# Kernel tuning notes

Measured on AMD Instinct MI355X. Metric: run time of the kernel, lower is better.

## Reference

```python
import jax, jax.numpy as jnp
import numpy as np

B, O, A, H, Z = 4096, 512, 64, 2048, 256
CLAMP = 10.0


def _lin(x, w, b):
    # torch nn.Linear layout: w [out, in]
    return x @ w.T + b


def setup_inputs() -> dict:
    key = jax.random.key(0)
    ks = jax.random.split(key, 24)
    n = jax.random.normal
    s = 0.02
    inp = {
        'x_t': n(ks[0], (B, O), jnp.float32),
        'a_prev': n(ks[1], (B, A), jnp.float32),
        'h_prev': n(ks[2], (B, H), jnp.float32),
        'eps': n(ks[3], (B, Z), jnp.float32),
        # prior_net: Linear(H,H) -> ReLU -> Linear(H, 2Z)
        'prior_w1': n(ks[4], (H, H), jnp.float32) * s,
        'prior_b1': jnp.zeros((H,), jnp.float32),
        'prior_w2': n(ks[5], (2 * Z, H), jnp.float32) * s,
        'prior_b2': jnp.zeros((2 * Z,), jnp.float32),
        # enc_net: Linear(O+H,H) -> ReLU -> Linear(H, 2Z)
        'enc_w1': n(ks[6], (H, O + H), jnp.float32) * s,
        'enc_b1': jnp.zeros((H,), jnp.float32),
        'enc_w2': n(ks[7], (2 * Z, H), jnp.float32) * s,
        'enc_b2': jnp.zeros((2 * Z,), jnp.float32),
        # dec_net: Linear(Z+H,H) -> ReLU -> Linear(H, 2O)
        'dec_w1': n(ks[8], (H, Z + H), jnp.float32) * s,
        'dec_b1': jnp.zeros((H,), jnp.float32),
        'dec_w2': n(ks[9], (2 * O, H), jnp.float32) * s,
        'dec_b2': jnp.zeros((2 * O,), jnp.float32),
        # GRUCell: input = O + A + Z, gates ordered (r, z, n)
        'w_ih': n(ks[10], (3 * H, O + A + Z), jnp.float32) * s,
        'w_hh': n(ks[11], (3 * H, H), jnp.float32) * s,
        'b_ih': jnp.zeros((3 * H,), jnp.float32),
        'b_hh': jnp.zeros((3 * H,), jnp.float32),
    }
    return inp


def vrnn_step(x_t, a_prev, h_prev, eps,
              prior_w1, prior_b1, prior_w2, prior_b2,
              enc_w1, enc_b1, enc_w2, enc_b2,
              dec_w1, dec_b1, dec_w2, dec_b2,
              w_ih, w_hh, b_ih, b_hh):
    # prior stats from h_prev
    prior_stats = _lin(jax.nn.relu(_lin(h_prev, prior_w1, prior_b1)), prior_w2, prior_b2)
    mu_p, logvar_p = jnp.split(prior_stats, 2, axis=-1)

    # encoder on [x, h]
    enc_stats = _lin(jax.nn.relu(_lin(jnp.concatenate([x_t, h_prev], -1), enc_w1, enc_b1)), enc_w2, enc_b2)
    mu_q, logvar_q = jnp.split(enc_stats, 2, axis=-1)
    logvar_q = jnp.clip(logvar_q, -CLAMP, CLAMP)
    std_q = jnp.exp(0.5 * logvar_q)
    z_t = mu_q + eps * std_q  # reparameterization

    # decoder on [z, h]
    dec_out = _lin(jax.nn.relu(_lin(jnp.concatenate([z_t, h_prev], -1), dec_w1, dec_b1)), dec_w2, dec_b2)
    mu_x, logvar_x = jnp.split(dec_out, 2, axis=-1)
    logvar_x = jnp.clip(logvar_x, -CLAMP, CLAMP)
    nll = 0.5 * jnp.sum((x_t - mu_x) ** 2 * jnp.exp(-logvar_x) + logvar_x, axis=-1)

    # KL(q || p), diagonal Gaussians
    var_p = jnp.exp(logvar_p)
    kl = 0.5 * jnp.sum((mu_q - mu_p) ** 2 / var_p + jnp.exp(logvar_q) / var_p
                       + (logvar_p - logvar_q) - 1.0, axis=-1)

    # GRUCell (torch gate order: r, z, n)
    rnn_in = jnp.concatenate([x_t, z_t, a_prev], -1)
    gi = rnn_in @ w_ih.T + b_ih
    gh = h_prev @ w_hh.T + b_hh
    i_r, i_z, i_n = jnp.split(gi, 3, axis=-1)
    h_r, h_z, h_n = jnp.split(gh, 3, axis=-1)
    r = jax.nn.sigmoid(i_r + h_r)
    zg = jax.nn.sigmoid(i_z + h_z)
    n = jnp.tanh(i_n + r * h_n)
    h_t = (1.0 - zg) * n + zg * h_prev

    return h_t, nll, kl, z_t, mu_q, logvar_q


def reference(x_t, a_prev, h_prev, eps,
              prior_w1, prior_b1, prior_w2, prior_b2,
              enc_w1, enc_b1, enc_w2, enc_b2,
              dec_w1, dec_b1, dec_w2, dec_b2,
              w_ih, w_hh, b_ih, b_hh):
    return vrnn_step(x_t, a_prev, h_prev, eps,
                     prior_w1, prior_b1, prior_w2, prior_b2,
                     enc_w1, enc_b1, enc_w2, enc_b2,
                     dec_w1, dec_b1, dec_w2, dec_b2,
                     w_ih, w_hh, b_ih, b_hh)
```

## Files before the change

### kernel.cpp

```cpp
#include <hip/hip_runtime.h>
#include <stdint.h>


#define B_SZ 4096
#define H_SZ 2048
#define Z_SZ 256

typedef __attribute__((ext_vector_type(4))) float f32x4;
typedef __attribute__((ext_vector_type(8))) short s16x8;

__device__ __forceinline__ uint16_t f2b(float f) {
  union { float f; uint32_t u; } v; v.f = f;
  uint32_t u = v.u;
  uint32_t r = (u + 0x7FFFu + ((u >> 16) & 1u)) >> 16;
  return (uint16_t)r;
}
__device__ __forceinline__ float b2f(uint16_t h) {
  union { uint32_t u; float f; } v; v.u = ((uint32_t)h) << 16; return v.f;
}
__device__ __forceinline__ float clip10(float v) { return fminf(fmaxf(v, -10.0f), 10.0f); }

struct MC {
  const float* src[11];
  uint16_t* dst[11];
  int c8[11];
  int sld[11];
  int dld[11];
  int base[12];
};

__global__ __launch_bounds__(256) void multiconv(MC mc, int nseg, int total) {
  int gid = blockIdx.x * 256 + threadIdx.x;
  if (gid >= total) return;
  int s = 0;
  while (s + 1 < nseg && gid >= mc.base[s + 1]) ++s;
  int local = gid - mc.base[s];
  int c8 = mc.c8[s];
  int row = local / c8;
  int cg = local - row * c8;
  const f32x4* sp = (const f32x4*)(mc.src[s] + (size_t)row * mc.sld[s] + (size_t)cg * 8);
  f32x4 lo = sp[0], hi = sp[1];
  s16x8 p;
  p[0] = (short)f2b(lo[0]); p[1] = (short)f2b(lo[1]);
  p[2] = (short)f2b(lo[2]); p[3] = (short)f2b(lo[3]);
  p[4] = (short)f2b(hi[0]); p[5] = (short)f2b(hi[1]);
  p[6] = (short)f2b(hi[2]); p[7] = (short)f2b(hi[3]);
  *(s16x8*)(mc.dst[s] + (size_t)row * mc.dld[s] + (size_t)cg * 8) = p;
}

__device__ __forceinline__ void gload_lds16(const uint16_t* g, uint16_t* l) {
  __builtin_amdgcn_global_load_lds(
      (const __attribute__((address_space(1))) uint32_t*)g,
      (__attribute__((address_space(3))) uint32_t*)(uintptr_t)(void*)l,
      16, 0, 0);
}

__global__ __launch_bounds__(512, 2)
void gemm8p(const uint16_t* __restrict__ A, int lda,
            const uint16_t* __restrict__ W,
            const float* __restrict__ bias0, const float* __restrict__ bias1,
            uint16_t* __restrict__ C0, int ldc0, int splitN,
            uint16_t* __restrict__ C1, int ldc1,
            int Nt, int K) {
  __shared__ uint16_t Ab[2][2][8192];
  __shared__ uint16_t Bb[2][2][8192];
  const int NT = K >> 6;
  int mtile = blockIdx.x / Nt;
  int ntile = blockIdx.x - mtile * Nt;
  const int brow = mtile << 8, bcol = ntile << 8;
  const int tid = threadIdx.x;
  const int l = tid & 63;
  const int w = tid >> 6;
  const int wr = w >> 2, wcn = w & 3;
  const int fr = l & 15, fq = l >> 4;
  const int sr0 = tid >> 3;
  const int scg = tid & 7;
  const int dstoff = tid * 8;

  f32x4 acc[8][4] = {};

  auto stage_half = [&](int t, int q, int d) {
#pragma unroll
    for (int r = 0; r < 2; ++r) {
      int row = r * 64 + sr0;
      int col = (scg ^ (row & 7)) << 3;
      if (q < 2)
        gload_lds16(A + (size_t)(brow + q * 128 + row) * lda + t * 64 + col,
                    &Ab[d][q][r * 4096 + dstoff]);
      else
        gload_lds16(W + (size_t)(bcol + (q - 2) * 128 + row) * K + t * 64 + col,
                    &Bb[d][q - 2][r * 4096 + dstoff]);
    }
  };

#pragma unroll
  for (int q = 0; q < 4; ++q) stage_half(0, q, 0);

  for (int t = 0; t < NT; ++t) {
    const int d = t & 1;
    const bool more = (t + 1 < NT);
    if (more) {
      stage_half(t + 1, 0, d ^ 1);
      asm volatile("s_waitcnt vmcnt(2)" ::: "memory");
    } else {
      asm volatile("s_waitcnt vmcnt(0)" ::: "memory");
    }
    __builtin_amdgcn_s_barrier();

#pragma unroll
    for (int q = 0; q < 4; ++q) {
      const int mh = q >> 1, nh = q & 1;
      if (q > 0 && more) stage_half(t + 1, q, d ^ 1);
      s16x8 fb[2][2];
#pragma unroll
      for (int nn = 0; nn < 2; ++nn)
#pragma unroll
        for (int ks = 0; ks < 2; ++ks) {
          int row = wcn * 64 + nh * 32 + nn * 16 + fr;
          int half = row >> 7, rl = row & 127;
          fb[nn][ks] = *(const s16x8*)&Bb[d][half]
              [rl * 64 + ((ks * 32 + fq * 8) ^ ((rl & 7) << 3))];
        }
      s16x8 fa[4][2];
#pragma unroll
      for (int mm = 0; mm < 4; ++mm)
#pragma unroll
        for (int ks = 0; ks < 2; ++ks) {
          int rl = mh * 64 + mm * 16 + fr;
          fa[mm][ks] = *(const s16x8*)&Ab[d][wr]
              [rl * 64 + ((ks * 32 + fq * 8) ^ ((rl & 7) << 3))];
        }
      __builtin_amdgcn_s_setprio(1);
#pragma unroll
      for (int mm = 0; mm < 4; ++mm)
#pragma unroll
        for (int nn = 0; nn < 2; ++nn)
#pragma unroll
          for (int ks = 0; ks < 2; ++ks)
            acc[mh * 4 + mm][nh * 2 + nn] = __builtin_amdgcn_mfma_f32_16x16x32_bf16(
                fa[mm][ks], fb[nn][ks], acc[mh * 4 + mm][nh * 2 + nn], 0, 0, 0);
      __builtin_amdgcn_s_setprio(0);
      __builtin_amdgcn_s_barrier();
    }
  }

#pragma unroll
  for (int m = 0; m < 8; ++m) {
    int grow = brow + wr * 128 + m * 16 + fq * 4;
#pragma unroll
    for (int n = 0; n < 4; ++n) {
      int gcol = bcol + wcn * 64 + n * 16 + fr;
      bool first = gcol < splitN;
      float bs = first ? bias0[gcol] : bias1[gcol - splitN];
#pragma unroll
      for (int i = 0; i < 4; ++i) {
        float v = acc[m][n][i] + bs;
        if (first) {
          C0[(size_t)(grow + i) * ldc0 + gcol] = f2b(fmaxf(v, 0.0f));
        } else {
          C1[(size_t)(grow + i) * ldc1 + (gcol - splitN)] = f2b(v);
        }
      }
    }
  }
}

template <int EPI>
__global__ __launch_bounds__(256)
void gemm_bt(const uint16_t* __restrict__ A0, int lda0, int ks1,
             const uint16_t* __restrict__ A1, int lda1, int ks2,
             const uint16_t* __restrict__ A2, int lda2,
             const uint16_t* __restrict__ W,
             const float* __restrict__ bias0, const float* __restrict__ bias1,
             uint16_t* __restrict__ C0, int ldc0, int splitN,
             uint16_t* __restrict__ C1, int ldc1,
             int Nt, int K) {
  __shared__ uint16_t As[128 * 64];
  __shared__ uint16_t Ws[128 * 64];
  int mtile = blockIdx.x / Nt;
  int ntile = blockIdx.x - mtile * Nt;
  const int row0 = mtile << 7, col0 = ntile << 7;
  const int t = threadIdx.x;
  const int w = t >> 6, l = t & 63;
  const int wr = w >> 1, wc = w & 1;
  const int sr = l >> 3, scg = l & 7;
  const int fr = l & 15, fq = l >> 4;

  f32x4 acc[4][4] = {};

  const uint16_t* Wbase = W + (size_t)(col0 + w * 32 + sr) * K + scg * 8;

  for (int k0 = 0; k0 < K; k0 += 64) {
    const uint16_t* ab; int ald, koff;
    if (k0 < ks1)      { ab = A0; ald = lda0; koff = k0; }
    else if (k0 < ks2) { ab = A1; ald = lda1; koff = k0 - ks1; }
    else               { ab = A2; ald = lda2; koff = k0 - ks2; }
    const uint16_t* Abase = ab + (size_t)(row0 + w * 32 + sr) * ald + koff + scg * 8;
#pragma unroll
    for (int j = 0; j < 4; ++j)
      gload_lds16(Abase + (size_t)(j * 8) * ald, &As[(w * 32 + j * 8) * 64]);
#pragma unroll
    for (int j = 0; j < 4; ++j)
      gload_lds16(Wbase + (size_t)(j * 8) * K + k0, &Ws[(w * 32 + j * 8) * 64]);
    __syncthreads();
#pragma unroll
    for (int ks = 0; ks < 2; ++ks) {
      s16x8 fa[4], fb[4];
#pragma unroll
      for (int m = 0; m < 4; ++m)
        fa[m] = *(const s16x8*)&As[(wr * 64 + m * 16 + fr) * 64 + ks * 32 + fq * 8];
#pragma unroll
      for (int n = 0; n < 4; ++n)
        fb[n] = *(const s16x8*)&Ws[(wc * 64 + n * 16 + fr) * 64 + ks * 32 + fq * 8];
#pragma unroll
      for (int m = 0; m < 4; ++m)
#pragma unroll
        for (int n = 0; n < 4; ++n)
          acc[m][n] = __builtin_amdgcn_mfma_f32_16x16x32_bf16(fa[m], fb[n], acc[m][n], 0, 0, 0);
    }
    __syncthreads();
  }

#pragma unroll
  for (int m = 0; m < 4; ++m) {
    int grow = row0 + wr * 64 + m * 16 + fq * 4;
#pragma unroll
    for (int n = 0; n < 4; ++n) {
      int gcol = col0 + wc * 64 + n * 16 + fr;
      bool first = (EPI != 3) || (gcol < splitN);
      float bs = first ? bias0[gcol] : bias1[gcol - splitN];
#pragma unroll
      for (int i = 0; i < 4; ++i) {
        float v = acc[m][n][i] + bs;
        if (EPI == 1 || (EPI == 3 && first)) v = fmaxf(v, 0.0f);
        if (first)
          C0[(size_t)(grow + i) * ldc0 + gcol] = f2b(v);
        else
          C1[(size_t)(grow + i) * ldc1 + (gcol - splitN)] = f2b(v);
      }
    }
  }
}

__global__ __launch_bounds__(256)
void gemm_ks(const uint16_t* __restrict__ A, int lda,
             const uint16_t* __restrict__ W, int Wld,
             float* __restrict__ P, int N,
             int Nt, int Khalf) {
  __shared__ uint16_t As[128 * 64];
  __shared__ uint16_t Ws[128 * 64];
  int bg = gridDim.x >> 1;
  int half = blockIdx.x >= bg;
  int bid = blockIdx.x - half * bg;
  int mtile = bid / Nt;
  int ntile = bid - mtile * Nt;
  const int row0 = mtile << 7, col0 = ntile << 7;
  const int t = threadIdx.x;
  const int w = t >> 6, l = t & 63;
  const int wr = w >> 1, wc = w & 1;
  const int sr = l >> 3, scg = l & 7;
  const int fr = l & 15, fq = l >> 4;

  f32x4 acc[4][4] = {};

  const uint16_t* Ab = A + half * Khalf;
  const uint16_t* Wb = W + half * Khalf;
  const uint16_t* Wbase = Wb + (size_t)(col0 + w * 32 + sr) * Wld + scg * 8;
  const uint16_t* Abase0 = Ab + (size_t)(row0 + w * 32 + sr) * lda + scg * 8;

  for (int k0 = 0; k0 < Khalf; k0 += 64) {
#pragma unroll
    for (int j = 0; j < 4; ++j)
      gload_lds16(Abase0 + (size_t)(j * 8) * lda + k0, &As[(w * 32 + j * 8) * 64]);
#pragma unroll
    for (int j = 0; j < 4; ++j)
      gload_lds16(Wbase + (size_t)(j * 8) * Wld + k0, &Ws[(w * 32 + j * 8) * 64]);
    __syncthreads();
#pragma unroll
    for (int ks = 0; ks < 2; ++ks) {
      s16x8 fa[4], fb[4];
#pragma unroll
      for (int m = 0; m < 4; ++m)
        fa[m] = *(const s16x8*)&As[(wr * 64 + m * 16 + fr) * 64 + ks * 32 + fq * 8];
#pragma unroll
      for (int n = 0; n < 4; ++n)
        fb[n] = *(const s16x8*)&Ws[(wc * 64 + n * 16 + fr) * 64 + ks * 32 + fq * 8];
#pragma unroll
      for (int m = 0; m < 4; ++m)
#pragma unroll
        for (int n = 0; n < 4; ++n)
          acc[m][n] = __builtin_amdgcn_mfma_f32_16x16x32_bf16(fa[m], fb[n], acc[m][n], 0, 0, 0);
    }
    __syncthreads();
  }

  float* Pf = P + (size_t)half * B_SZ * N;
#pragma unroll
  for (int m = 0; m < 4; ++m) {
    int grow = row0 + wr * 64 + m * 16 + fq * 4;
#pragma unroll
    for (int n = 0; n < 4; ++n) {
      int gcol = col0 + wc * 64 + n * 16 + fr;
#pragma unroll
      for (int i = 0; i < 4; ++i)
        Pf[(size_t)(grow + i) * N + gcol] = acc[m][n][i];
    }
  }
}

__global__ __launch_bounds__(256)
void combine2(const float* __restrict__ P, const float* __restrict__ bias,
              uint16_t* __restrict__ dst, int N, int total4) {
  int i = blockIdx.x * 256 + threadIdx.x;
  if (i >= total4) return;
  size_t idx = (size_t)i * 4;
  const float* P1 = P + (size_t)B_SZ * N;
  f32x4 a = *(const f32x4*)(P + idx);
  f32x4 b = *(const f32x4*)(P1 + idx);
  int col = (int)(idx & (size_t)(N - 1));
#pragma unroll
  for (int k = 0; k < 4; ++k)
    dst[idx + k] = f2b(a[k] + b[k] + bias[col + k]);
}

__global__ void z_kernel_t1(const uint16_t* __restrict__ es, const float* __restrict__ eps,
                            float* __restrict__ oz, float* __restrict__ omu,
                            float* __restrict__ olq, uint16_t* __restrict__ zbuf) {
  int i = blockIdx.x * 256 + threadIdx.x;
  int b = i >> 8, j = i & 255;
  float mu = b2f(es[(size_t)b * 512 + j]);
  float lq = clip10(b2f(es[(size_t)b * 512 + 256 + j]));
  float z = mu + eps[i] * __expf(0.5f * lq);
  oz[i] = z; omu[i] = mu; olq[i] = lq;
  zbuf[i] = f2b(z);
}

__device__ __forceinline__ float block_sum256(float v) {
  __shared__ float ps[4];
#pragma unroll
  for (int o = 32; o > 0; o >>= 1) v += __shfl_xor(v, o, 64);
  int l = threadIdx.x & 63, w = threadIdx.x >> 6;
  if (l == 0) ps[w] = v;
  __syncthreads();
  float r = ps[0] + ps[1] + ps[2] + ps[3];
  __syncthreads();
  return r;
}

__global__ __launch_bounds__(256)
void gru_fused_t1(const uint16_t* __restrict__ gi, int ldgi,
                  const uint16_t* __restrict__ gh, int ldgh,
                  const float* __restrict__ hp, const float* __restrict__ x,
                  const uint16_t* __restrict__ dec, const uint16_t* __restrict__ pst,
                  const uint16_t* __restrict__ es,
                  float* __restrict__ out_h, float* __restrict__ out_nll,
                  float* __restrict__ out_kl) {
  int b = blockIdx.x, t = threadIdx.x;
  size_t gbi = (size_t)b * ldgi + (size_t)t * 8;
  size_t gbh = (size_t)b * ldgh + (size_t)t * 8;
  s16x8 ir = *(const s16x8*)(gi + gbi);
  s16x8 iz = *(const s16x8*)(gi + gbi + 2048);
  s16x8 inn = *(const s16x8*)(gi + gbi + 4096);
  s16x8 hr = *(const s16x8*)(gh + gbh);
  s16x8 hz = *(const s16x8*)(gh + gbh + 2048);
  s16x8 hn = *(const s16x8*)(gh + gbh + 4096);
  size_t hbase = (size_t)b * 2048 + (size_t)t * 8;
  f32x4 h0 = *(const f32x4*)(hp + hbase);
  f32x4 h1v = *(const f32x4*)(hp + hbase + 4);
  f32x4 o0, o1;
#pragma unroll
  for (int e = 0; e < 8; ++e) {
    float r = 1.f / (1.f + __expf(-(b2f((uint16_t)ir[e]) + b2f((uint16_t)hr[e]))));
    float zg = 1.f / (1.f + __expf(-(b2f((uint16_t)iz[e]) + b2f((uint16_t)hz[e]))));
    float nv = b2f((uint16_t)inn[e]) + r * b2f((uint16_t)hn[e]);
    float t2 = __expf(-2.f * fabsf(nv));
    float n = (1.f - t2) / (1.f + t2);
    n = (nv >= 0.f) ? n : -n;
    float hv = (e < 4) ? h0[e] : h1v[e - 4];
    float o = (1.f - zg) * n + zg * hv;
    if (e < 4) o0[e] = o; else o1[e - 4] = o;
  }
  *(f32x4*)(out_h + hbase) = o0;
  *(f32x4*)(out_h + hbase + 4) = o1;

  float s = 0.f;
#pragma unroll
  for (int rr = 0; rr < 2; ++rr) {
    int j = t + rr * 256;
    float mu = b2f(dec[(size_t)b * 1024 + j]);
    float lx = clip10(b2f(dec[(size_t)b * 1024 + 512 + j]));
    float d = x[(size_t)b * 512 + j] - mu;
    s += d * d * __expf(-lx) + lx;
  }
  s = block_sum256(s);
  if (t == 0) out_nll[b] = 0.5f * s;

  float mu_p = b2f(pst[(size_t)b * 512 + t]);
  float lp = b2f(pst[(size_t)b * 512 + 256 + t]);
  float mu_q = b2f(es[(size_t)b * 512 + t]);
  float lq = clip10(b2f(es[(size_t)b * 512 + 256 + t]));
  float dq = mu_q - mu_p;
  float enl = __expf(-lp);
  float kv = dq * dq * enl + __expf(lq) * enl + (lp - lq) - 1.0f;
  kv = block_sum256(kv);
  if (t == 0) out_kl[b] = 0.5f * kv;
}

template <int MODE>
__global__ __launch_bounds__(256)
void gemm_nv(const float* __restrict__ A0, int ld0, int s1,
             const float* __restrict__ A1, int ld1, int s2,
             const float* __restrict__ A2, int ld2,
             const float* __restrict__ W, const float* __restrict__ bias,
             float* __restrict__ C, int N, int K) {
  int nb = N >> 8;
  int m = blockIdx.x / nb;
  int n = (blockIdx.x - m * nb) * 256 + threadIdx.x;
  const float* w = W + (size_t)n * K;
  float acc = 0.f;
  int k = 0;
  for (; k < s1; ++k) acc += A0[(size_t)m * ld0 + k] * w[k];
  for (; k < s2; ++k) acc += A1[(size_t)m * ld1 + (k - s1)] * w[k];
  for (; k < K; ++k) acc += A2[(size_t)m * ld2 + (k - s2)] * w[k];
  acc += bias[n];
  if (MODE == 1) acc = fmaxf(acc, 0.f);
  C[(size_t)m * N + n] = acc;
}

__global__ void z_nv(const float* __restrict__ ests, const float* __restrict__ eps,
                     float* __restrict__ oz, float* __restrict__ omu,
                     float* __restrict__ olq, float* __restrict__ zs, int row0, int nR) {
  int i = blockIdx.x * 256 + threadIdx.x;
  if (i >= nR * 256) return;
  int bl = i >> 8, j = i & 255;
  size_t g = (size_t)(row0 + bl) * 256 + j;
  float mu = ests[(size_t)bl * 512 + j];
  float lq = clip10(ests[(size_t)bl * 512 + 256 + j]);
  float z = mu + eps[g] * __expf(0.5f * lq);
  oz[g] = z; omu[g] = mu; olq[g] = lq;
  zs[(size_t)bl * 256 + j] = z;
}

__global__ void nll_nv(const float* __restrict__ x, const float* __restrict__ decs,
                       float* __restrict__ out, int row0) {
  int bl = blockIdx.x, l = threadIdx.x;
  int gb = row0 + bl;
  float s = 0.f;
  for (int j = l; j < 512; j += 64) {
    float mu = decs[(size_t)bl * 1024 + j];
    float lx = clip10(decs[(size_t)bl * 1024 + 512 + j]);
    float d = x[(size_t)gb * 512 + j] - mu;
    s += d * d * __expf(-lx) + lx;
  }
#pragma unroll
  for (int o = 32; o > 0; o >>= 1) s += __shfl_xor(s, o, 64);
  if (l == 0) out[gb] = 0.5f * s;
}

__global__ void kl_nv(const float* __restrict__ psts, const float* __restrict__ ests,
                      float* __restrict__ out, int row0) {
  int bl = blockIdx.x, l = threadIdx.x;
  int gb = row0 + bl;
  float s = 0.f;
  for (int j = l; j < 256; j += 64) {
    float mu_p = psts[(size_t)bl * 512 + j];
    float lp = psts[(size_t)bl * 512 + 256 + j];
    float mu_q = ests[(size_t)bl * 512 + j];
    float lq = clip10(ests[(size_t)bl * 512 + 256 + j]);
    float d = mu_q - mu_p;
    float enl = __expf(-lp);
    s += d * d * enl + __expf(lq) * enl + (lp - lq) - 1.0f;
  }
#pragma unroll
  for (int o = 32; o > 0; o >>= 1) s += __shfl_xor(s, o, 64);
  if (l == 0) out[gb] = 0.5f * s;
}

__global__ void gru_nv(const float* __restrict__ gis, const float* __restrict__ ghs,
                       const float* __restrict__ hp, float* __restrict__ ho,
                       int row0, int nR) {
  int i = blockIdx.x * 256 + threadIdx.x;
  if (i >= nR * 2048) return;
  int bl = i >> 11, j = i & 2047;
  size_t lb = (size_t)bl * 6144 + j;
  float r = 1.f / (1.f + __expf(-(gis[lb] + ghs[lb])));
  float zg = 1.f / (1.f + __expf(-(gis[lb + 2048] + ghs[lb + 2048])));
  float nv = gis[lb + 4096] + r * ghs[lb + 4096];
  float t2 = __expf(-2.f * fabsf(nv));
  float n = (1.f - t2) / (1.f + t2);
  n = (nv >= 0.f) ? n : -n;
  size_t g = (size_t)(row0 + bl) * 2048 + j;
  ho[g] = (1.f - zg) * n + zg * hp[g];
}

extern "C" void kernel_launch(void* const* d_in, const int* in_sizes, int n_in,
                              void* d_out, int out_size, void* d_ws, size_t ws_size,
                              hipStream_t stream) {
  const float* x_t = (const float*)d_in[0];
  const float* a_prev = (const float*)d_in[1];
  const float* h_prev = (const float*)d_in[2];
  const float* eps = (const float*)d_in[3];
  const float* prior_w1 = (const float*)d_in[4];
  const float* prior_b1 = (const float*)d_in[5];
  const float* prior_w2 = (const float*)d_in[6];
  const float* prior_b2 = (const float*)d_in[7];
  const float* enc_w1 = (const float*)d_in[8];
  const float* enc_b1 = (const float*)d_in[9];
  const float* enc_w2 = (const float*)d_in[10];
  const float* enc_b2 = (const float*)d_in[11];
  const float* dec_w1 = (const float*)d_in[12];
  const float* dec_b1 = (const float*)d_in[13];
  const float* dec_w2 = (const float*)d_in[14];
  const float* dec_b2 = (const float*)d_in[15];
  const float* w_ih = (const float*)d_in[16];
  const float* w_hh = (const float*)d_in[17];
  const float* b_ih = (const float*)d_in[18];
  const float* b_hh = (const float*)d_in[19];

  float* out = (float*)d_out;
  float* out_h = out;
  float* out_nll = out + (size_t)B_SZ * H_SZ;
  float* out_kl = out_nll + B_SZ;
  float* out_z = out_kl + B_SZ;
  float* out_mu = out_z + (size_t)B_SZ * Z_SZ;
  float* out_lq = out_mu + (size_t)B_SZ * Z_SZ;

  char* ws = (char*)d_ws;
  size_t off = 0;
  auto alloc = [&](size_t bytes) {
    void* p = ws + off;
    off += (bytes + 255) & ~(size_t)255;
    return p;
  };

  const size_t T1_DEMAND = 179600000;

  if (ws_size >= T1_DEMAND) {
    uint16_t* wcat = (uint16_t*)alloc((size_t)8192 * 2048 * 2);
    uint16_t* pw2 = (uint16_t*)alloc((size_t)512 * 2048 * 2);
    uint16_t* ew1 = (uint16_t*)alloc((size_t)2048 * 2560 * 2);
    uint16_t* ew2 = (uint16_t*)alloc((size_t)512 * 2048 * 2);
    uint16_t* dw1 = (uint16_t*)alloc((size_t)2048 * 2304 * 2);
    uint16_t* dw2 = (uint16_t*)alloc((size_t)1024 * 2048 * 2);
    uint16_t* wih = (uint16_t*)alloc((size_t)6144 * 832 * 2);
    uint16_t* xh = (uint16_t*)alloc((size_t)B_SZ * 2560 * 2);
    uint16_t* zbuf = (uint16_t*)alloc((size_t)B_SZ * 256 * 2);
    uint16_t* abuf = (uint16_t*)alloc((size_t)B_SZ * 64 * 2);
    uint16_t* h1 = (uint16_t*)alloc((size_t)B_SZ * 2048 * 2);
    uint16_t* pstats = (uint16_t*)alloc((size_t)B_SZ * 512 * 2);
    uint16_t* estats = (uint16_t*)alloc((size_t)B_SZ * 512 * 2);
    uint16_t* decout = (uint16_t*)alloc((size_t)B_SZ * 1024 * 2);
    uint16_t* gh = (uint16_t*)alloc((size_t)B_SZ * 6144 * 2);
    float* Pbuf = (float*)wcat;
    uint16_t* gi = wcat;

    MC mc;
    int nseg = 0, acc = 0;
    auto seg = [&](const float* s, uint16_t* d, int R, int C, int sld, int dld) {
      mc.src[nseg] = s; mc.dst[nseg] = d; mc.c8[nseg] = C / 8;
      mc.sld[nseg] = sld; mc.dld[nseg] = dld; mc.base[nseg] = acc;
      acc += R * (C / 8); ++nseg;
    };
    seg(prior_w1, wcat, 2048, 2048, 2048, 2048);
    seg(w_hh, wcat + (size_t)2048 * 2048, 6144, 2048, 2048, 2048);
    seg(prior_w2, pw2, 512, 2048, 2048, 2048);
    seg(enc_w1, ew1, 2048, 2560, 2560, 2560);
    seg(enc_w2, ew2, 512, 2048, 2048, 2048);
    seg(dec_w1, dw1, 2048, 2304, 2304, 2304);
    seg(dec_w2, dw2, 1024, 2048, 2048, 2048);
    seg(w_ih, wih, 6144, 832, 832, 832);
    seg(x_t, xh, B_SZ, 512, 512, 2560);
    seg(h_prev, xh + 512, B_SZ, 2048, 2048, 2560);
    seg(a_prev, abuf, B_SZ, 64, 64, 64);
    mc.base[nseg] = acc;
    multiconv<<<dim3((acc + 255) / 256), dim3(256), 0, stream>>>(mc, nseg, acc);

    gemm8p<<<dim3((B_SZ / 256) * 32), dim3(512), 0, stream>>>(
        xh + 512, 2560, wcat, prior_b1, b_hh, h1, 2048, 2048, gh, 6144, 32, 2048);
    gemm_ks<<<dim3((B_SZ / 128) * 4 * 2), dim3(256), 0, stream>>>(
        h1, 2048, pw2, 2048, Pbuf, 512, 4, 1024);
    combine2<<<dim3(B_SZ * 512 / 4 / 256), dim3(256), 0, stream>>>(
        Pbuf, prior_b2, pstats, 512, B_SZ * 512 / 4);
    gemm_bt<1><<<dim3((B_SZ / 128) * 16), dim3(256), 0, stream>>>(
        xh, 2560, 2560, xh, 2560, 2560, xh, 2560, ew1,
        enc_b1, enc_b1, h1, 2048, 2048, h1, 2048, 16, 2560);
    gemm_ks<<<dim3((B_SZ / 128) * 4 * 2), dim3(256), 0, stream>>>(
        h1, 2048, ew2, 2048, Pbuf, 512, 4, 1024);
    combine2<<<dim3(B_SZ * 512 / 4 / 256), dim3(256), 0, stream>>>(
        Pbuf, enc_b2, estats, 512, B_SZ * 512 / 4);
    z_kernel_t1<<<dim3(B_SZ * Z_SZ / 256), dim3(256), 0, stream>>>(
        estats, eps, out_z, out_mu, out_lq, zbuf);
    gemm_bt<1><<<dim3((B_SZ / 128) * 16), dim3(256), 0, stream>>>(
        zbuf, 256, 256, xh + 512, 2560, 2304, xh, 2560, dw1,
        dec_b1, dec_b1, h1, 2048, 2048, h1, 2048, 16, 2304);
    gemm_ks<<<dim3((B_SZ / 128) * 8 * 2), dim3(256), 0, stream>>>(
        h1, 2048, dw2, 2048, Pbuf, 1024, 8, 1024);
    combine2<<<dim3(B_SZ * 1024 / 4 / 256), dim3(256), 0, stream>>>(
        Pbuf, dec_b2, decout, 1024, B_SZ * 1024 / 4);
    gemm_bt<2><<<dim3((B_SZ / 128) * 48), dim3(256), 0, stream>>>(
        xh, 2560, 512, zbuf, 256, 768, abuf, 64, wih,
        b_ih, b_ih, gi, 6144, 6144, gi, 6144, 48, 832);
    gru_fused_t1<<<dim3(B_SZ), dim3(256), 0, stream>>>(
        gi, 6144, gh, 6144, h_prev, x_t, decout, pstats, estats,
        out_h, out_nll, out_kl);
  } else {
    int R = 512;
    while (R > 32 && (size_t)R * 66560 + 4096 > ws_size) R >>= 1;
    float* h1s = (float*)alloc((size_t)R * 2048 * 4);
    float* psts = (float*)alloc((size_t)R * 512 * 4);
    float* ests = (float*)alloc((size_t)R * 512 * 4);
    float* decs = (float*)alloc((size_t)R * 1024 * 4);
    float* zs = (float*)alloc((size_t)R * 256 * 4);
    float* gis = (float*)alloc((size_t)R * 6144 * 4);
    float* ghs = (float*)alloc((size_t)R * 6144 * 4);
    const float* dummy = x_t;

    auto nv = [&](const float* A0, int ld0, int s1, const float* A1, int ld1, int s2,
                  const float* A2, int ld2, const float* W, const float* bias,
                  float* C, int M, int N, int K, int relu) {
      dim3 grid(M * (N / 256));
      if (relu)
        gemm_nv<1><<<grid, dim3(256), 0, stream>>>(A0, ld0, s1, A1, ld1, s2, A2, ld2, W, bias, C, N, K);
      else
        gemm_nv<0><<<grid, dim3(256), 0, stream>>>(A0, ld0, s1, A1, ld1, s2, A2, ld2, W, bias, C, N, K);
    };

    for (int s = 0; s < B_SZ / R; ++s) {
      int r0 = s * R;
      const float* xs = x_t + (size_t)r0 * 512;
      const float* hs = h_prev + (size_t)r0 * 2048;
      const float* as = a_prev + (size_t)r0 * 64;
      nv(hs, 2048, 2048, dummy, 0, 2048, dummy, 0, prior_w1, prior_b1, h1s, R, 2048, 2048, 1);
      nv(h1s, 2048, 2048, dummy, 0, 2048, dummy, 0, prior_w2, prior_b2, psts, R, 512, 2048, 0);
      nv(xs, 512, 512, hs, 2048, 2560, dummy, 0, enc_w1, enc_b1, h1s, R, 2048, 2560, 1);
      nv(h1s, 2048, 2048, dummy, 0, 2048, dummy, 0, enc_w2, enc_b2, ests, R, 512, 2048, 0);
      z_nv<<<dim3((R * 256 + 255) / 256), dim3(256), 0, stream>>>(
          ests, eps, out_z, out_mu, out_lq, zs, r0, R);
      nv(zs, 256, 256, hs, 2048, 2304, dummy, 0, dec_w1, dec_b1, h1s, R, 2048, 2304, 1);
      nv(h1s, 2048, 2048, dummy, 0, 2048, dummy, 0, dec_w2, dec_b2, decs, R, 1024, 2048, 0);
      nv(hs, 2048, 2048, dummy, 0, 2048, dummy, 0, w_hh, b_hh, ghs, R, 6144, 2048, 0);
      nv(xs, 512, 512, zs, 256, 768, as, 64, w_ih, b_ih, gis, R, 6144, 832, 0);
      nll_nv<<<dim3(R), dim3(64), 0, stream>>>(x_t, decs, out_nll, r0);
      kl_nv<<<dim3(R), dim3(64), 0, stream>>>(psts, ests, out_kl, r0);
      gru_nv<<<dim3((R * 2048 + 255) / 256), dim3(256), 0, stream>>>(
          gis, ghs, h_prev, out_h, r0, R);
    }
  }
}
```

Baseline: 488.4 us.

## Fold h_prev parts of encoder and decoder first layers into one mega GEMM

The h_prev-dependent columns of enc_w1 and dec_w1 are appended to the prior_w1/w_hh weight concat, so one large GEMM over h_prev produces prior hidden, GRU gh, and partial encoder/decoder pre-activations (N=12288). The encoder and decoder first-layer GEMMs then only cover their x (K=512) and z (K=256) parts, and a new epilogue adds the stored partial sum before applying ReLU. This removes the redundant K=2048 h_prev work from two GEMMs, at the cost of rounding the partial sums to bf16 between passes, a larger intermediate buffer, an extra bias-concat kernel, and workspace aliasing.

```diff
diff --git a/kernel.cpp b/kernel.cpp
--- a/kernel.cpp
+++ b/kernel.cpp
@@ -21,12 +21,12 @@
 __device__ __forceinline__ float clip10(float v) { return fminf(fmaxf(v, -10.0f), 10.0f); }
 
 struct MC {
-  const float* src[11];
-  uint16_t* dst[11];
-  int c8[11];
-  int sld[11];
-  int dld[11];
-  int base[12];
+  const float* src[14];
+  uint16_t* dst[14];
+  int c8[14];
+  int sld[14];
+  int dld[14];
+  int base[15];
 };
 
 __global__ __launch_bounds__(256) void multiconv(MC mc, int nseg, int total) {
@@ -48,6 +48,18 @@
   *(s16x8*)(mc.dst[s] + (size_t)row * mc.dld[s] + (size_t)cg * 8) = p;
 }
 
+__global__ void biascat_kernel(const float* __restrict__ b0, const float* __restrict__ b1,
+                               const float* __restrict__ b2, const float* __restrict__ b3,
+                               float* __restrict__ dst) {
+  int j = blockIdx.x * 256 + threadIdx.x;
+  float v;
+  if (j < 2048) v = b0[j];
+  else if (j < 8192) v = b1[j - 2048];
+  else if (j < 10240) v = b2[j - 8192];
+  else v = b3[j - 10240];
+  dst[j] = v;
+}
+
 __device__ __forceinline__ void gload_lds16(const uint16_t* g, uint16_t* l) {
   __builtin_amdgcn_global_load_lds(
       (const __attribute__((address_space(1))) uint32_t*)g,
@@ -58,9 +70,8 @@
 __global__ __launch_bounds__(512, 2)
 void gemm8p(const uint16_t* __restrict__ A, int lda,
             const uint16_t* __restrict__ W,
-            const float* __restrict__ bias0, const float* __restrict__ bias1,
-            uint16_t* __restrict__ C0, int ldc0, int splitN,
-            uint16_t* __restrict__ C1, int ldc1,
+            const float* __restrict__ bias,
+            uint16_t* __restrict__ C, int ldc, int splitN,
             int Nt, int K) {
   __shared__ uint16_t Ab[2][2][8192];
   __shared__ uint16_t Bb[2][2][8192];
@@ -150,16 +161,13 @@
 #pragma unroll
     for (int n = 0; n < 4; ++n) {
       int gcol = bcol + wcn * 64 + n * 16 + fr;
-      bool first = gcol < splitN;
-      float bs = first ? bias0[gcol] : bias1[gcol - splitN];
+      float bs = bias[gcol];
+      bool doRelu = gcol < splitN;
 #pragma unroll
       for (int i = 0; i < 4; ++i) {
         float v = acc[m][n][i] + bs;
-        if (first) {
-          C0[(size_t)(grow + i) * ldc0 + gcol] = f2b(fmaxf(v, 0.0f));
-        } else {
-          C1[(size_t)(grow + i) * ldc1 + (gcol - splitN)] = f2b(v);
-        }
+        if (doRelu) v = fmaxf(v, 0.0f);
+        C[(size_t)(grow + i) * ldc + gcol] = f2b(v);
       }
     }
   }
@@ -231,12 +239,18 @@
       float bs = first ? bias0[gcol] : bias1[gcol - splitN];
 #pragma unroll
       for (int i = 0; i < 4; ++i) {
-        float v = acc[m][n][i] + bs;
-        if (EPI == 1 || (EPI == 3 && first)) v = fmaxf(v, 0.0f);
-        if (first)
-          C0[(size_t)(grow + i) * ldc0 + gcol] = f2b(v);
-        else
-          C1[(size_t)(grow + i) * ldc1 + (gcol - splitN)] = f2b(v);
+        size_t idx0 = (size_t)(grow + i) * ldc0 + gcol;
+        if (EPI == 6) {
+          float v6 = acc[m][n][i] + b2f(C0[idx0]);
+          C0[idx0] = f2b(fmaxf(v6, 0.0f));
+        } else {
+          float v = acc[m][n][i] + bs;
+          if (EPI == 1 || (EPI == 3 && first)) v = fmaxf(v, 0.0f);
+          if (first)
+            C0[idx0] = f2b(v);
+          else
+            C1[(size_t)(grow + i) * ldc1 + (gcol - splitN)] = f2b(v);
+        }
       }
     }
   }
@@ -533,26 +547,27 @@
     return p;
   };
 
-  const size_t T1_DEMAND = 179600000;
+  const size_t T1_DEMAND = 194297856;
 
   if (ws_size >= T1_DEMAND) {
-    uint16_t* wcat = (uint16_t*)alloc((size_t)8192 * 2048 * 2);
+    uint16_t* wmega = (uint16_t*)alloc((size_t)12288 * 2048 * 2);
+    uint16_t* wih = (uint16_t*)alloc((size_t)6144 * 832 * 2);
+    uint16_t* wx_enc = (uint16_t*)alloc((size_t)2048 * 512 * 2);
+    uint16_t* wz_dec = (uint16_t*)alloc((size_t)2048 * 256 * 2);
     uint16_t* pw2 = (uint16_t*)alloc((size_t)512 * 2048 * 2);
-    uint16_t* ew1 = (uint16_t*)alloc((size_t)2048 * 2560 * 2);
     uint16_t* ew2 = (uint16_t*)alloc((size_t)512 * 2048 * 2);
-    uint16_t* dw1 = (uint16_t*)alloc((size_t)2048 * 2304 * 2);
     uint16_t* dw2 = (uint16_t*)alloc((size_t)1024 * 2048 * 2);
-    uint16_t* wih = (uint16_t*)alloc((size_t)6144 * 832 * 2);
-    uint16_t* xh = (uint16_t*)alloc((size_t)B_SZ * 2560 * 2);
-    uint16_t* zbuf = (uint16_t*)alloc((size_t)B_SZ * 256 * 2);
+    uint16_t* xbuf = (uint16_t*)alloc((size_t)B_SZ * 512 * 2);
+    uint16_t* hbuf = (uint16_t*)alloc((size_t)B_SZ * 2048 * 2);
     uint16_t* abuf = (uint16_t*)alloc((size_t)B_SZ * 64 * 2);
-    uint16_t* h1 = (uint16_t*)alloc((size_t)B_SZ * 2048 * 2);
-    uint16_t* pstats = (uint16_t*)alloc((size_t)B_SZ * 512 * 2);
-    uint16_t* estats = (uint16_t*)alloc((size_t)B_SZ * 512 * 2);
-    uint16_t* decout = (uint16_t*)alloc((size_t)B_SZ * 1024 * 2);
-    uint16_t* gh = (uint16_t*)alloc((size_t)B_SZ * 6144 * 2);
-    float* Pbuf = (float*)wcat;
-    uint16_t* gi = wcat;
+    uint16_t* megaC = (uint16_t*)alloc((size_t)B_SZ * 12288 * 2);
+    float* biascat = (float*)alloc(12288 * 4);
+    float* Pbuf = (float*)wmega;
+    uint16_t* gi = wmega;
+    uint16_t* pstats = hbuf;
+    uint16_t* estats = hbuf + (size_t)2097152;
+    uint16_t* zbuf = hbuf + (size_t)4194304;
+    uint16_t* decout = pw2;
 
     MC mc;
     int nseg = 0, acc = 0;
@@ -561,47 +576,50 @@
       mc.sld[nseg] = sld; mc.dld[nseg] = dld; mc.base[nseg] = acc;
       acc += R * (C / 8); ++nseg;
     };
-    seg(prior_w1, wcat, 2048, 2048, 2048, 2048);
-    seg(w_hh, wcat + (size_t)2048 * 2048, 6144, 2048, 2048, 2048);
+    seg(prior_w1, wmega, 2048, 2048, 2048, 2048);
+    seg(w_hh, wmega + (size_t)2048 * 2048, 6144, 2048, 2048, 2048);
+    seg(enc_w1 + 512, wmega + (size_t)8192 * 2048, 2048, 2048, 2560, 2048);
+    seg(dec_w1 + 256, wmega + (size_t)10240 * 2048, 2048, 2048, 2304, 2048);
+    seg(enc_w1, wx_enc, 2048, 512, 2560, 512);
+    seg(dec_w1, wz_dec, 2048, 256, 2304, 256);
     seg(prior_w2, pw2, 512, 2048, 2048, 2048);
-    seg(enc_w1, ew1, 2048, 2560, 2560, 2560);
     seg(enc_w2, ew2, 512, 2048, 2048, 2048);
-    seg(dec_w1, dw1, 2048, 2304, 2304, 2304);
     seg(dec_w2, dw2, 1024, 2048, 2048, 2048);
     seg(w_ih, wih, 6144, 832, 832, 832);
-    seg(x_t, xh, B_SZ, 512, 512, 2560);
-    seg(h_prev, xh + 512, B_SZ, 2048, 2048, 2560);
+    seg(x_t, xbuf, B_SZ, 512, 512, 512);
+    seg(h_prev, hbuf, B_SZ, 2048, 2048, 2048);
     seg(a_prev, abuf, B_SZ, 64, 64, 64);
     mc.base[nseg] = acc;
     multiconv<<<dim3((acc + 255) / 256), dim3(256), 0, stream>>>(mc, nseg, acc);
-
-    gemm8p<<<dim3((B_SZ / 256) * 32), dim3(512), 0, stream>>>(
-        xh + 512, 2560, wcat, prior_b1, b_hh, h1, 2048, 2048, gh, 6144, 32, 2048);
+    biascat_kernel<<<dim3(48), dim3(256), 0, stream>>>(prior_b1, b_hh, enc_b1, dec_b1, biascat);
+
+    gemm8p<<<dim3((B_SZ / 256) * 48), dim3(512), 0, stream>>>(
+        hbuf, 2048, wmega, biascat, megaC, 12288, 2048, 48, 2048);
     gemm_ks<<<dim3((B_SZ / 128) * 4 * 2), dim3(256), 0, stream>>>(
-        h1, 2048, pw2, 2048, Pbuf, 512, 4, 1024);
+        megaC, 12288, pw2, 2048, Pbuf, 512, 4, 1024);
     combine2<<<dim3(B_SZ * 512 / 4 / 256), dim3(256), 0, stream>>>(
         Pbuf, prior_b2, pstats, 512, B_SZ * 512 / 4);
-    gemm_bt<1><<<dim3((B_SZ / 128) * 16), dim3(256), 0, stream>>>(
-        xh, 2560, 2560, xh, 2560, 2560, xh, 2560, ew1,
-        enc_b1, enc_b1, h1, 2048, 2048, h1, 2048, 16, 2560);
+    gemm_bt<6><<<dim3((B_SZ / 128) * 16), dim3(256), 0, stream>>>(
+        xbuf, 512, 512, xbuf, 512, 512, xbuf, 512, wx_enc,
+        enc_b1, enc_b1, megaC + 8192, 12288, 2048, megaC + 8192, 12288, 16, 512);
     gemm_ks<<<dim3((B_SZ / 128) * 4 * 2), dim3(256), 0, stream>>>(
-        h1, 2048, ew2, 2048, Pbuf, 512, 4, 1024);
+        megaC + 8192, 12288, ew2, 2048, Pbuf, 512, 4, 1024);
     combine2<<<dim3(B_SZ * 512 / 4 / 256), dim3(256), 0, stream>>>(
         Pbuf, enc_b2, estats, 512, B_SZ * 512 / 4);
     z_kernel_t1<<<dim3(B_SZ * Z_SZ / 256), dim3(256), 0, stream>>>(
         estats, eps, out_z, out_mu, out_lq, zbuf);
-    gemm_bt<1><<<dim3((B_SZ / 128) * 16), dim3(256), 0, stream>>>(
-        zbuf, 256, 256, xh + 512, 2560, 2304, xh, 2560, dw1,
-        dec_b1, dec_b1, h1, 2048, 2048, h1, 2048, 16, 2304);
+    gemm_bt<6><<<dim3((B_SZ / 128) * 16), dim3(256), 0, stream>>>(
+        zbuf, 256, 256, zbuf, 256, 256, zbuf, 256, wz_dec,
+        dec_b1, dec_b1, megaC + 10240, 12288, 2048, megaC + 10240, 12288, 16, 256);
     gemm_ks<<<dim3((B_SZ / 128) * 8 * 2), dim3(256), 0, stream>>>(
-        h1, 2048, dw2, 2048, Pbuf, 1024, 8, 1024);
+        megaC + 10240, 12288, dw2, 2048, Pbuf, 1024, 8, 1024);
     combine2<<<dim3(B_SZ * 1024 / 4 / 256), dim3(256), 0, stream>>>(
         Pbuf, dec_b2, decout, 1024, B_SZ * 1024 / 4);
     gemm_bt<2><<<dim3((B_SZ / 128) * 48), dim3(256), 0, stream>>>(
-        xh, 2560, 512, zbuf, 256, 768, abuf, 64, wih,
+        xbuf, 512, 512, zbuf, 256, 768, abuf, 64, wih,
         b_ih, b_ih, gi, 6144, 6144, gi, 6144, 48, 832);
     gru_fused_t1<<<dim3(B_SZ), dim3(256), 0, stream>>>(
-        gi, 6144, gh, 6144, h_prev, x_t, decout, pstats, estats,
+        gi, 6144, megaC + 2048, 12288, h_prev, x_t, decout, pstats, estats,
         out_h, out_nll, out_kl);
   } else {
     int R = 512;
```

Measured after the change: 483.4 us. No clear change (-1.0%).
